# Performance work log

Hardware: AMD Instinct MI355X
Metric: run time of the kernel (lower is better)

The kernel has to match this reference:

```python
import jax, jax.numpy as jnp
import numpy as np

B, S, D, DK, DV = 4, 4096, 1024, 64, 64


def setup_inputs() -> dict:
    rng = jax.random.key(0)
    k1, k2, k3, k4, k5, k6 = jax.random.split(rng, 6)
    query = jax.random.normal(k1, (B, S, D), dtype=jnp.float32)
    key = jax.random.normal(k2, (B, S, D), dtype=jnp.float32)
    value = jax.random.normal(k3, (B, S, D), dtype=jnp.float32)
    Wq = jax.random.normal(k4, (D, DK), dtype=jnp.float32)
    Wk = jax.random.normal(k5, (D, DK), dtype=jnp.float32)
    Wv = jax.random.normal(k6, (D, DV), dtype=jnp.float32)
    mask = jnp.tril(jnp.ones((S, S), dtype=jnp.bool_))  # causal mask, broadcasts over batch
    return {"query": query, "key": key, "value": value,
            "Wq": Wq, "Wk": Wk, "Wv": Wv, "mask": mask}


def reference(query, key, value, Wq, Wk, Wv, mask):
    # linear projections: [B,S,D] @ [D,dk] -> [B,S,dk]
    q = jnp.matmul(query, Wq)
    k = jnp.matmul(key, Wk)
    v = jnp.matmul(value, Wv)
    scale = 1.0 / jnp.sqrt(jnp.asarray(DK, dtype=q.dtype))
    # scores: [B,S,S]
    attn = jnp.einsum("bqd,bkd->bqk", q, k) * scale
    attn = jnp.where(mask, attn, -jnp.inf)  # mask==0 -> -inf
    attn = jax.nn.softmax(attn, axis=-1)
    x = jnp.matmul(attn, v)  # [B,S,dv]
    return x
```

## Files before the change

kernel.cpp:

```cpp
#include <hip/hip_runtime.h>
#include <math.h>


#define SEQ 4096
#define DIM 1024
#define HD  64
#define NB  4
#define NSPLIT 4

typedef __attribute__((ext_vector_type(4))) float    f32x4;
typedef __attribute__((ext_vector_type(8))) _Float16 f16x8;
typedef __attribute__((ext_vector_type(4))) _Float16 f16x4;

#define MFMA16 __builtin_amdgcn_mfma_f32_16x16x32_f16

__device__ __forceinline__ int SW(int row, int k) {
  return row * 64 + (k ^ ((row & 7) << 3));
}

__global__ __launch_bounds__(256) void wsplit_kernel(
    const float* __restrict__ Wq, const float* __restrict__ Wk,
    const float* __restrict__ Wv, _Float16* __restrict__ wf)
{
  const int which = blockIdx.x;
  const int kt    = blockIdx.y;
  const float* __restrict__ W = (which == 0) ? Wq : (which == 1) ? Wk : Wv;
  const float scale = (which == 0) ? 0.18033688011112042f : 1.0f;
  const size_t tb = ((size_t)which * 16 + kt) * 8192;
#pragma unroll
  for (int i = 0; i < 2; ++i) {
    const int pair = threadIdx.x + 256 * i;
    const int lane = pair & 63, f = pair >> 6;
    const int ks = f >> 2, ct = f & 3;
    const int col = ct * 16 + (lane & 15);
    const int k0 = kt * 64 + ks * 32 + (lane >> 4) * 8;
    f16x8 hv, lv;
#pragma unroll
    for (int j = 0; j < 8; ++j) {
      const float y = W[(size_t)(k0 + j) * HD + col] * scale;
      const _Float16 h = (_Float16)y;
      hv[j] = h;
      lv[j] = (_Float16)(y - (float)h);
    }
    *(f16x8*)&wf[tb + (size_t)f * 512 + lane * 8]       = hv;
    *(f16x8*)&wf[tb + (size_t)(8 + f) * 512 + lane * 8] = lv;
  }
}

__global__ __launch_bounds__(256, 3) void proj_kernel(
    const float* __restrict__ Xq, const float* __restrict__ Xk,
    const float* __restrict__ Xv,
    const _Float16* __restrict__ wf,
    _Float16* __restrict__ qh, _Float16* __restrict__ ql,
    _Float16* __restrict__ kh, _Float16* __restrict__ kl,
    _Float16* __restrict__ vt)
{
  __shared__ __attribute__((aligned(16))) float    Xs[2][64 * 32];
  __shared__ __attribute__((aligned(16))) _Float16 Ws[2][4096];

  const int which = blockIdx.y;
  const float* __restrict__ X = (which == 0) ? Xq : (which == 1) ? Xk : Xv;

  const int t = threadIdx.x, lane = t & 63, w = t >> 6;
  const int bm = blockIdx.x * 64;

  const int xrow = t >> 2;
  const int xc   = (t & 3) * 2;
  const float* gX = X + (size_t)(bm + xrow) * DIM + xc * 4;
  const int xd0 = xrow * 32 + ((xc ^ (xrow & 7)) * 4);
  const int xd1 = xrow * 32 + (((xc + 1) ^ (xrow & 7)) * 4);

  const int wr = t >> 7;
  const int wi = (t & 127) * 16;
  const _Float16* gW = wf + (size_t)which * 131072 + wr * 4096 + wi;
  const int wd = wr * 2048 + wi;

  const int frow = lane & 15;
  const int ldsrow = w * 16 + frow;
  const int kc = (lane >> 4) * 2;
  const int xr0 = ldsrow * 32 + ((kc ^ (ldsrow & 7)) * 4);
  const int xr1 = ldsrow * 32 + (((kc + 1) ^ (ldsrow & 7)) * 4);

  f32x4 acc[4] = {{0,0,0,0},{0,0,0,0},{0,0,0,0},{0,0,0,0}};
  f32x4 xg0, xg1;
  f16x8 wg0, wg1;

  auto loadTile = [&](int st) {
    const float* xb = gX + st * 32;
    xg0 = *(const f32x4*)(xb);
    xg1 = *(const f32x4*)(xb + 4);
    const _Float16* wb = gW + (st >> 1) * 8192 + (st & 1) * 2048;
    wg0 = *(const f16x8*)(wb);
    wg1 = *(const f16x8*)(wb + 8);
  };

  loadTile(0);
#pragma unroll 1
  for (int st = 0; st < 32; ++st) {
    const int buf = st & 1;
    asm volatile("s_waitcnt vmcnt(0)" ::: "memory");
    __builtin_amdgcn_sched_barrier(0);
    *(f32x4*)&Xs[buf][xd0] = xg0;
    *(f32x4*)&Xs[buf][xd1] = xg1;
    *(f16x8*)&Ws[buf][wd]     = wg0;
    *(f16x8*)&Ws[buf][wd + 8] = wg1;
    if (st + 1 < 32) loadTile(st + 1);
    asm volatile("s_waitcnt lgkmcnt(0)" ::: "memory");
    __builtin_amdgcn_sched_barrier(0);
    __builtin_amdgcn_s_barrier();
    __builtin_amdgcn_sched_barrier(0);

    f32x4 x0 = *(const f32x4*)&Xs[buf][xr0];
    f32x4 x1 = *(const f32x4*)&Xs[buf][xr1];
    f16x8 xh, xl;
#pragma unroll
    for (int j = 0; j < 4; ++j) {
      const _Float16 h0 = (_Float16)x0[j];
      xh[j] = h0; xl[j] = (_Float16)(x0[j] - (float)h0);
      const _Float16 h1 = (_Float16)x1[j];
      xh[j + 4] = h1; xl[j + 4] = (_Float16)(x1[j] - (float)h1);
    }
#pragma unroll
    for (int ct = 0; ct < 4; ++ct) {
      f16x8 bh = *(const f16x8*)&Ws[buf][ct * 512 + lane * 8];
      f16x8 bl = *(const f16x8*)&Ws[buf][2048 + ct * 512 + lane * 8];
      acc[ct] = MFMA16(xh, bh, acc[ct], 0, 0, 0);
      acc[ct] = MFMA16(xl, bh, acc[ct], 0, 0, 0);
      acc[ct] = MFMA16(xh, bl, acc[ct], 0, 0, 0);
    }
  }

  const size_t orow0 = (size_t)bm + w * 16 + (lane >> 4) * 4;
  if (which < 2) {
    _Float16* oh = (which == 0) ? qh : kh;
    _Float16* ol = (which == 0) ? ql : kl;
#pragma unroll
    for (int ct = 0; ct < 4; ++ct)
#pragma unroll
      for (int r = 0; r < 4; ++r) {
        const float y = acc[ct][r];
        const _Float16 h = (_Float16)y;
        const size_t idx = (orow0 + r) * HD + ct * 16 + (lane & 15);
        oh[idx] = h;
        ol[idx] = (_Float16)(y - (float)h);
      }
  } else {
    const int batch = (int)(orow0 >> 12);
    const int pos = (int)(orow0 & 4095);
#pragma unroll
    for (int ct = 0; ct < 4; ++ct) {
      f16x4 hv;
#pragma unroll
      for (int r = 0; r < 4; ++r) hv[r] = (_Float16)acc[ct][r];
      *(f16x4*)&vt[((size_t)batch * HD + ct * 16 + (lane & 15)) * SEQ + pos] = hv;
    }
  }
}

__global__ __launch_bounds__(256) void attn_kernel(
    const _Float16* __restrict__ qh, const _Float16* __restrict__ ql,
    const _Float16* __restrict__ kh, const _Float16* __restrict__ kl,
    const _Float16* __restrict__ vt,
    _Float16* __restrict__ opart, float* __restrict__ mlp)
{
  __shared__ __attribute__((aligned(16))) _Float16 Ksh[64 * 64];
  __shared__ __attribute__((aligned(16))) _Float16 Ksl[64 * 64];
  __shared__ __attribute__((aligned(16))) _Float16 Vs [64 * 64];
  __shared__ __attribute__((aligned(16))) _Float16 Pt [64 * 64];

  const int t = threadIdx.x, lane = t & 63, w = t >> 6;
  const int b = blockIdx.y;
  const int p = blockIdx.x >> 2, s = blockIdx.x & 3;
  const size_t bS = (size_t)b * SEQ;

  for (int sel = 0; sel < 2; ++sel) {
    const int qb = sel ? (63 - p) : p;
    const int qrow0 = qb * 64 + w * 16;
    const int nt = (qb >= s) ? ((qb - s) >> 2) + 1 : 0;

    float m[4] = {-INFINITY, -INFINITY, -INFINITY, -INFINITY};
    float lsum[4] = {0.f, 0.f, 0.f, 0.f};
    f32x4 o[4] = {{0,0,0,0},{0,0,0,0},{0,0,0,0},{0,0,0,0}};

    if (nt > 0) {
      const _Float16* qhp = qh + (bS + qrow0 + (lane & 15)) * HD + ((lane >> 4) * 8);
      const _Float16* qlp = ql + (bS + qrow0 + (lane & 15)) * HD + ((lane >> 4) * 8);
      f16x8 qhf[2], qlf[2];
      qhf[0] = *(const f16x8*)(qhp);      qhf[1] = *(const f16x8*)(qhp + 32);
      qlf[0] = *(const f16x8*)(qlp);      qlf[1] = *(const f16x8*)(qlp + 32);

      for (int i = 0; i < nt; ++i) {
        const int kt = s + 4 * i;
        const int j0 = kt * 64;

        __syncthreads();
#pragma unroll
        for (int c = 0; c < 2; ++c) {
          const int lin = t + 256 * c;
          const int row = lin >> 3, d8 = (lin & 7) * 8;
          const int dst = SW(row, d8);
          *(f16x8*)&Ksh[dst] = *(const f16x8*)&kh[(bS + j0 + row) * HD + d8];
          *(f16x8*)&Ksl[dst] = *(const f16x8*)&kl[(bS + j0 + row) * HD + d8];
          *(f16x8*)&Vs[dst]  = *(const f16x8*)&vt[((size_t)b * HD + row) * SEQ + j0 + d8];
        }
        __syncthreads();

        f32x4 sacc[4] = {{0,0,0,0},{0,0,0,0},{0,0,0,0},{0,0,0,0}};
#pragma unroll
        for (int kk = 0; kk < 2; ++kk)
#pragma unroll
          for (int kt4 = 0; kt4 < 4; ++kt4) {
            const int ba = SW(kt4 * 16 + (lane & 15), kk * 32 + (lane >> 4) * 8);
            f16x8 bh = *(const f16x8*)&Ksh[ba];
            f16x8 bl = *(const f16x8*)&Ksl[ba];
            sacc[kt4] = MFMA16(qhf[kk], bh, sacc[kt4], 0, 0, 0);
            sacc[kt4] = MFMA16(qlf[kk], bh, sacc[kt4], 0, 0, 0);
            sacc[kt4] = MFMA16(qhf[kk], bl, sacc[kt4], 0, 0, 0);
          }

        if (kt == qb) {
#pragma unroll
          for (int kt4 = 0; kt4 < 4; ++kt4) {
            const int key = j0 + kt4 * 16 + (lane & 15);
#pragma unroll
            for (int r = 0; r < 4; ++r)
              if (key > qrow0 + (lane >> 4) * 4 + r) sacc[kt4][r] = -INFINITY;
          }
        }

        float alf[4];
#pragma unroll
        for (int r = 0; r < 4; ++r) {
          float mx = fmaxf(fmaxf(sacc[0][r], sacc[1][r]),
                           fmaxf(sacc[2][r], sacc[3][r]));
          mx = fmaxf(mx, __shfl_xor(mx, 1));
          mx = fmaxf(mx, __shfl_xor(mx, 2));
          mx = fmaxf(mx, __shfl_xor(mx, 4));
          mx = fmaxf(mx, __shfl_xor(mx, 8));
          const float mn = fmaxf(m[r], mx);
          const float al = exp2f(m[r] - mn);
          const int prow = w * 16 + (lane >> 4) * 4 + r;
          float ps = 0.f;
#pragma unroll
          for (int kt4 = 0; kt4 < 4; ++kt4) {
            const _Float16 ph = (_Float16)exp2f(sacc[kt4][r] - mn);
            ps += (float)ph;
            Pt[SW(prow, kt4 * 16 + (lane & 15))] = ph;
          }
          ps += __shfl_xor(ps, 1);
          ps += __shfl_xor(ps, 2);
          ps += __shfl_xor(ps, 4);
          ps += __shfl_xor(ps, 8);
          lsum[r] = lsum[r] * al + ps;
          m[r] = mn;
          alf[r] = al;
        }
        const f32x4 av = {alf[0], alf[1], alf[2], alf[3]};
#pragma unroll
        for (int ct = 0; ct < 4; ++ct) o[ct] *= av;

#pragma unroll
        for (int kk = 0; kk < 2; ++kk) {
          f16x8 pa = *(const f16x8*)&Pt[SW(w * 16 + (lane & 15),
                                           kk * 32 + (lane >> 4) * 8)];
#pragma unroll
          for (int ct = 0; ct < 4; ++ct) {
            f16x8 vb = *(const f16x8*)&Vs[SW(ct * 16 + (lane & 15),
                                             kk * 32 + (lane >> 4) * 8)];
            o[ct] = MFMA16(pa, vb, o[ct], 0, 0, 0);
          }
        }
      }
    }

    f32x4 invv;
#pragma unroll
    for (int r = 0; r < 4; ++r) invv[r] = (nt > 0) ? 1.0f / lsum[r] : 0.0f;
    const size_t ridx0 = (size_t)(b * NSPLIT + s) * SEQ + qrow0 + (lane >> 4) * 4;
#pragma unroll
    for (int ct = 0; ct < 4; ++ct)
#pragma unroll
      for (int r = 0; r < 4; ++r)
        opart[(ridx0 + r) * HD + ct * 16 + (lane & 15)] =
            (_Float16)(o[ct][r] * invv[r]);
    if ((lane & 15) == 0) {
#pragma unroll
      for (int r = 0; r < 4; ++r) {
        mlp[(ridx0 + r) * 2]     = m[r];
        mlp[(ridx0 + r) * 2 + 1] = lsum[r];
      }
    }
  }
}

__global__ __launch_bounds__(256) void combine_kernel(
    const _Float16* __restrict__ opart, const float* __restrict__ mlp,
    float* __restrict__ out)
{
  const int g = blockIdx.x * 256 + threadIdx.x;
  const int row = g >> 4;
  const int cq = (g & 15) * 4;
  const int b = row >> 12, pos = row & 4095;

  float mv[4], lv[4], msx = -INFINITY;
#pragma unroll
  for (int s = 0; s < 4; ++s) {
    const size_t ri = (size_t)(b * NSPLIT + s) * SEQ + pos;
    mv[s] = mlp[ri * 2];
    lv[s] = mlp[ri * 2 + 1];
    msx = fmaxf(msx, mv[s]);
  }
  f32x4 num = {0.f, 0.f, 0.f, 0.f};
  float L = 0.f;
#pragma unroll
  for (int s = 0; s < 4; ++s) {
    const float wgt = lv[s] * exp2f(mv[s] - msx);
    L += wgt;
    const size_t ri = (size_t)(b * NSPLIT + s) * SEQ + pos;
    const f16x4 ov = *(const f16x4*)&opart[ri * HD + cq];
#pragma unroll
    for (int j = 0; j < 4; ++j) num[j] += wgt * (float)ov[j];
  }
  const float inv = 1.0f / L;
  f32x4 res = {num[0] * inv, num[1] * inv, num[2] * inv, num[3] * inv};
  *(f32x4*)&out[(size_t)row * HD + cq] = res;
}

extern "C" void kernel_launch(void* const* d_in, const int* in_sizes, int n_in,
                              void* d_out, int out_size, void* d_ws, size_t ws_size,
                              hipStream_t stream) {
  const float* query = (const float*)d_in[0];
  const float* key   = (const float*)d_in[1];
  const float* value = (const float*)d_in[2];
  const float* Wq    = (const float*)d_in[3];
  const float* Wk    = (const float*)d_in[4];
  const float* Wv    = (const float*)d_in[5];

  float* out = (float*)d_out;

  _Float16* qh  = (_Float16*)d_ws;
  _Float16* ql  = qh  + (size_t)NB * SEQ * HD;
  _Float16* kh  = ql  + (size_t)NB * SEQ * HD;
  _Float16* kl  = kh  + (size_t)NB * SEQ * HD;
  _Float16* vt  = kl  + (size_t)NB * SEQ * HD;
  _Float16* wf  = vt  + (size_t)NB * SEQ * HD;
  _Float16* opart = wf + (size_t)3 * 16 * 8192;
  float* mlp = (float*)(opart + (size_t)NB * NSPLIT * SEQ * HD);

  wsplit_kernel<<<dim3(3, 16), 256, 0, stream>>>(Wq, Wk, Wv, wf);
  proj_kernel<<<dim3(256, 3), 256, 0, stream>>>(query, key, value, wf,
                                                qh, ql, kh, kl, vt);
  attn_kernel<<<dim3(128, NB), 256, 0, stream>>>(qh, ql, kh, kl, vt, opart, mlp);
  combine_kernel<<<1024, 256, 0, stream>>>(opart, mlp, out);
}
```

Baseline: 89.62 us.

## Split projection K dimension across two blocks and reduce in a finish kernel

The projection GEMM is split-K into two halves along the 1024 input dimension, doubling the grid from 768 to 1536 blocks to fill more compute units. Partial fp32 results go to a workspace, and a new finish kernel sums them and performs the fp16 hi/lo split and the V transpose. The V transpose now goes through shared memory and is written with vectorized stores. The cost is an extra kernel launch and an fp32 round trip of the partial projections through global memory.

```diff
diff --git a/kernel.cpp b/kernel.cpp
--- a/kernel.cpp
+++ b/kernel.cpp
@@ -51,14 +51,13 @@
     const float* __restrict__ Xq, const float* __restrict__ Xk,
     const float* __restrict__ Xv,
     const _Float16* __restrict__ wf,
-    _Float16* __restrict__ qh, _Float16* __restrict__ ql,
-    _Float16* __restrict__ kh, _Float16* __restrict__ kl,
-    _Float16* __restrict__ vt)
+    float* __restrict__ Yp)
 {
   __shared__ __attribute__((aligned(16))) float    Xs[2][64 * 32];
   __shared__ __attribute__((aligned(16))) _Float16 Ws[2][4096];
 
-  const int which = blockIdx.y;
+  const int ksp   = blockIdx.y;
+  const int which = blockIdx.z;
   const float* __restrict__ X = (which == 0) ? Xq : (which == 1) ? Xk : Xv;
 
   const int t = threadIdx.x, lane = t & 63, w = t >> 6;
@@ -66,7 +65,7 @@
 
   const int xrow = t >> 2;
   const int xc   = (t & 3) * 2;
-  const float* gX = X + (size_t)(bm + xrow) * DIM + xc * 4;
+  const float* gX = X + (size_t)(bm + xrow) * DIM + ksp * 512 + xc * 4;
   const int xd0 = xrow * 32 + ((xc ^ (xrow & 7)) * 4);
   const int xd1 = xrow * 32 + (((xc + 1) ^ (xrow & 7)) * 4);
 
@@ -89,14 +88,15 @@
     const float* xb = gX + st * 32;
     xg0 = *(const f32x4*)(xb);
     xg1 = *(const f32x4*)(xb + 4);
-    const _Float16* wb = gW + (st >> 1) * 8192 + (st & 1) * 2048;
+    const _Float16* wb = gW + (size_t)((st >> 1) + ksp * 8) * 8192
+                             + (st & 1) * 2048;
     wg0 = *(const f16x8*)(wb);
     wg1 = *(const f16x8*)(wb + 8);
   };
 
   loadTile(0);
 #pragma unroll 1
-  for (int st = 0; st < 32; ++st) {
+  for (int st = 0; st < 16; ++st) {
     const int buf = st & 1;
     asm volatile("s_waitcnt vmcnt(0)" ::: "memory");
     __builtin_amdgcn_sched_barrier(0);
@@ -104,7 +104,7 @@
     *(f32x4*)&Xs[buf][xd1] = xg1;
     *(f16x8*)&Ws[buf][wd]     = wg0;
     *(f16x8*)&Ws[buf][wd + 8] = wg1;
-    if (st + 1 < 32) loadTile(st + 1);
+    if (st + 1 < 16) loadTile(st + 1);
     asm volatile("s_waitcnt lgkmcnt(0)" ::: "memory");
     __builtin_amdgcn_sched_barrier(0);
     __builtin_amdgcn_s_barrier();
@@ -131,29 +131,72 @@
   }
 
   const size_t orow0 = (size_t)bm + w * 16 + (lane >> 4) * 4;
+  float* yb = Yp + ((size_t)(ksp * 3 + which) * SEQ * NB) * HD;
+#pragma unroll
+  for (int ct = 0; ct < 4; ++ct)
+#pragma unroll
+    for (int r = 0; r < 4; ++r)
+      yb[(orow0 + r) * HD + ct * 16 + (lane & 15)] = acc[ct][r];
+}
+
+__global__ __launch_bounds__(256) void finish_kernel(
+    const float* __restrict__ Yp,
+    _Float16* __restrict__ qh, _Float16* __restrict__ ql,
+    _Float16* __restrict__ kh, _Float16* __restrict__ kl,
+    _Float16* __restrict__ vt)
+{
+  __shared__ float Vs[64 * 65];
+  const int which = blockIdx.y;
+  const int t = threadIdx.x;
+  const int row = t >> 2;
+  const int c0 = (t & 3) * 16;
+  const size_t rbase = (size_t)blockIdx.x * 64;
+  const float* y0 = Yp + ((size_t)(0 * 3 + which) * SEQ * NB) * HD;
+  const float* y1 = Yp + ((size_t)(1 * 3 + which) * SEQ * NB) * HD;
+
+  float s[16];
+#pragma unroll
+  for (int u = 0; u < 4; ++u) {
+    const size_t off = (rbase + row) * HD + c0 + u * 4;
+    f32x4 a = *(const f32x4*)(y0 + off);
+    f32x4 b = *(const f32x4*)(y1 + off);
+#pragma unroll
+    for (int j = 0; j < 4; ++j) s[u * 4 + j] = a[j] + b[j];
+  }
+
   if (which < 2) {
     _Float16* oh = (which == 0) ? qh : kh;
     _Float16* ol = (which == 0) ? ql : kl;
-#pragma unroll
-    for (int ct = 0; ct < 4; ++ct)
-#pragma unroll
-      for (int r = 0; r < 4; ++r) {
-        const float y = acc[ct][r];
-        const _Float16 h = (_Float16)y;
-        const size_t idx = (orow0 + r) * HD + ct * 16 + (lane & 15);
-        oh[idx] = h;
-        ol[idx] = (_Float16)(y - (float)h);
-      }
+    f16x8 hv0, hv1, lv0, lv1;
+#pragma unroll
+    for (int j = 0; j < 8; ++j) {
+      const _Float16 h0 = (_Float16)s[j];
+      hv0[j] = h0; lv0[j] = (_Float16)(s[j] - (float)h0);
+      const _Float16 h1 = (_Float16)s[8 + j];
+      hv1[j] = h1; lv1[j] = (_Float16)(s[8 + j] - (float)h1);
+    }
+    const size_t ob = (rbase + row) * HD + c0;
+    *(f16x8*)&oh[ob]     = hv0;
+    *(f16x8*)&oh[ob + 8] = hv1;
+    *(f16x8*)&ol[ob]     = lv0;
+    *(f16x8*)&ol[ob + 8] = lv1;
   } else {
-    const int batch = (int)(orow0 >> 12);
-    const int pos = (int)(orow0 & 4095);
-#pragma unroll
-    for (int ct = 0; ct < 4; ++ct) {
-      f16x4 hv;
-#pragma unroll
-      for (int r = 0; r < 4; ++r) hv[r] = (_Float16)acc[ct][r];
-      *(f16x4*)&vt[((size_t)batch * HD + ct * 16 + (lane & 15)) * SEQ + pos] = hv;
-    }
+#pragma unroll
+    for (int j = 0; j < 16; ++j) Vs[row * 65 + c0 + j] = s[j];
+    __syncthreads();
+    const int col = t >> 2;
+    const int p0 = (t & 3) * 16;
+    const int b = (int)(rbase >> 12);
+    const int pos = (int)(rbase & 4095) + p0;
+    f16x8 o0, o1;
+#pragma unroll
+    for (int j = 0; j < 8; ++j) {
+      o0[j] = (_Float16)Vs[(p0 + j) * 65 + col];
+      o1[j] = (_Float16)Vs[(p0 + 8 + j) * 65 + col];
+    }
+    _Float16* vb = vt + ((size_t)b * HD + col) * SEQ + pos;
+    *(f16x8*)(vb)     = o0;
+    *(f16x8*)(vb + 8) = o1;
   }
 }
 
@@ -346,10 +389,11 @@
   _Float16* wf  = vt  + (size_t)NB * SEQ * HD;
   _Float16* opart = wf + (size_t)3 * 16 * 8192;
   float* mlp = (float*)(opart + (size_t)NB * NSPLIT * SEQ * HD);
+  float* Yp  = mlp + (size_t)NB * NSPLIT * SEQ * 2;
 
   wsplit_kernel<<<dim3(3, 16), 256, 0, stream>>>(Wq, Wk, Wv, wf);
-  proj_kernel<<<dim3(256, 3), 256, 0, stream>>>(query, key, value, wf,
-                                                qh, ql, kh, kl, vt);
+  proj_kernel<<<dim3(256, 2, 3), 256, 0, stream>>>(query, key, value, wf, Yp);
+  finish_kernel<<<dim3(256, 3), 256, 0, stream>>>(Yp, qh, ql, kh, kl, vt);
   attn_kernel<<<dim3(128, NB), 256, 0, stream>>>(qh, ql, kh, kl, vt, opart, mlp);
   combine_kernel<<<1024, 256, 0, stream>>>(opart, mlp, out);
 }
```

Result: slower. 100.1 us (+11.6%).
